# Kernel tuning notes

Hardware: AMD Instinct MI355X
Metric: run time of the kernel (lower is better)

## Reference

```python
import jax, jax.numpy as jnp
import numpy as np

B, F, D = 16384, 32, 64   # batch, n_continuous_features, input_dim
H = 2 * D                  # hidden = 2*input_dim per the d_hidden spec


def setup_inputs() -> dict:
    key = jax.random.key(0)
    ks = jax.random.split(key, 6)
    s1 = 1.0 / np.sqrt(D).astype(np.float32)
    s2 = 1.0 / np.sqrt(H).astype(np.float32)
    return {
        "X": jax.random.normal(ks[0], (B, F), jnp.float32),
        "r_": jax.random.normal(ks[1], (B, F, D), jnp.float32),
        # stacked per-feature weights (one tiny MLP per continuous column)
        "W1": jax.random.normal(ks[2], (F, D, H), jnp.float32) * s1,
        "b1": jax.random.normal(ks[3], (F, H), jnp.float32) * s1,
        "W2": jax.random.normal(ks[4], (F, H, 1), jnp.float32) * s2,
        "b2": jax.random.normal(ks[5], (F, 1), jnp.float32) * s2,
    }


def reference(X, r_, W1, b1, W2, b2):
    # Per-feature 2-layer MLP (Linear->relu->Linear->relu), batched over the
    # feature axis instead of the original Python loop over ModuleDict.
    h = jax.nn.relu(jnp.einsum('bfd,fdh->bfh', r_, W1) + b1)   # [B,F,H]
    y = jax.nn.relu(jnp.einsum('bfh,fho->bfo', h, W2) + b2)    # [B,F,1]
    x = X[..., None]                                           # [B,F,1] raw scalar per column
    # Original returns list of (x_col, mlp_out) pairs; we pack them as [B,F,2]
    # with [...,0]=x and [...,1]=mlp output (same values, dense layout).
    return jnp.concatenate([x, y], axis=-1)
```

## Files before the change

### kernel.cpp

```cpp
#include <hip/hip_runtime.h>
#include <hip/hip_bf16.h>
#include <stdint.h>

#define B_SZ 16384
#define F_SZ 32
#define D_SZ 64
#define H_SZ 128
#define RSTRIDE 72

typedef __attribute__((ext_vector_type(8))) short  short8;
typedef __attribute__((ext_vector_type(4))) float  float4v;
typedef __attribute__((ext_vector_type(4))) unsigned int uint4v;

__device__ __forceinline__ unsigned int pkbf(float lo, float hi) {
  unsigned int ulo = __builtin_bit_cast(unsigned int, lo) + 0x8000u;
  unsigned int uhi = __builtin_bit_cast(unsigned int, hi) + 0x8000u;
  return __builtin_amdgcn_perm(uhi, ulo, 0x07060302u);
}

__global__ __launch_bounds__(256) void ContMlp_prep(
    const float* __restrict__ W1, const float* __restrict__ b1,
    const float* __restrict__ W2, unsigned short* __restrict__ w1t,
    unsigned int* __restrict__ bw) {
  const int f  = blockIdx.x >> 2;
  const int hq = blockIdx.x & 3;
  const int h0 = hq * 32;
  const int t  = threadIdx.x;
  __shared__ float lds[D_SZ][33];
  const float* w1f = W1 + (size_t)f * (D_SZ * H_SZ);
#pragma unroll
  for (int i = 0; i < 8; ++i) {
    int idx = t + 256 * i;
    int d = idx >> 5, hh = idx & 31;
    lds[d][hh] = w1f[d * H_SZ + h0 + hh];
  }
  __syncthreads();
  unsigned short* o = w1t + (size_t)f * (H_SZ * D_SZ);
#pragma unroll
  for (int i = 0; i < 8; ++i) {
    int idx = t + 256 * i;
    int hh = idx >> 6, d = idx & 63;
    unsigned int u = __builtin_bit_cast(unsigned int, lds[d][hh]) + 0x8000u;
    o[(h0 + hh) * D_SZ + d] = (unsigned short)(u >> 16);
  }
  if (hq == 0 && t < H_SZ) {
    unsigned int ub = __builtin_bit_cast(unsigned int, b1[f * H_SZ + t]) + 0x8000u;
    unsigned int uw = __builtin_bit_cast(unsigned int, W2[f * H_SZ + t]) + 0x8000u;
    bw[f * H_SZ + t] = (ub & 0xFFFF0000u) | (uw >> 16);
  }
}

__device__ __forceinline__ void compute_sub(
    float4v c0, float4v c1, float4v c2, float4v c3,
    const unsigned short* w1l, const unsigned int* bwl,
    float b2f, int col, int quad, float* store_ptr) {
  unsigned int p0 = pkbf(c0.x, c0.y), p1 = pkbf(c0.z, c0.w);
  unsigned int p2 = pkbf(c1.x, c1.y), p3 = pkbf(c1.z, c1.w);
  unsigned int p4 = pkbf(c2.x, c2.y), p5 = pkbf(c2.z, c2.w);
  unsigned int p6 = pkbf(c3.x, c3.y), p7 = pkbf(c3.z, c3.w);
  uint4v bq0 = {p0, p1, p2, p3};
  uint4v bq1 = {p4, p5, p6, p7};
  short8 bf0 = __builtin_bit_cast(short8, bq0);
  short8 bf1 = __builtin_bit_cast(short8, bq1);

  float ysum = 0.f;
#pragma unroll
  for (int t = 0; t < 8; ++t) {
    const unsigned short* wrow = w1l + (col + 16 * t) * RSTRIDE + quad * 8;
    short8 a0 = *(const short8*)(wrow);
    short8 a1 = *(const short8*)(wrow + 32);
    float4v acc = {0.f, 0.f, 0.f, 0.f};
    acc = __builtin_amdgcn_mfma_f32_16x16x32_bf16(a0, bf0, acc, 0, 0, 0);
    acc = __builtin_amdgcn_mfma_f32_16x16x32_bf16(a1, bf1, acc, 0, 0, 0);
    uint4v bwv = *(const uint4v*)(bwl + 16 * t + quad * 4);
#pragma unroll
    for (int r = 0; r < 4; ++r) {
      unsigned int u = bwv[r];
      float b1v = __builtin_bit_cast(float, u & 0xFFFF0000u);
      float w2v = __builtin_bit_cast(float, u << 16);
      ysum = fmaf(fmaxf(acc[r] + b1v, 0.f), w2v, ysum);
    }
  }
  ysum += __shfl_xor(ysum, 16, 64);
  ysum += __shfl_xor(ysum, 32, 64);
  float y = fmaxf(ysum + b2f, 0.f);
  if (quad == 0) *store_ptr = y;
}

__global__ void ContMlp_main(
    const float* __restrict__ r_,
    const unsigned short* __restrict__ w1t, const unsigned int* __restrict__ bw,
    const float* __restrict__ b2, float* __restrict__ ydst,
    int y_fmul, int y_rmul, int y_cadd) {
  const int f    = blockIdx.x & 31;
  const int tile = blockIdx.x >> 5;
  const int w    = threadIdx.x >> 6;
  const int l    = threadIdx.x & 63;
  const int col  = l & 15;
  const int quad = l >> 4;

  __shared__ unsigned short w1l[H_SZ * RSTRIDE];
  __shared__ unsigned int   bwl[H_SZ];

  {
    const uint4v* src = (const uint4v*)(w1t + (size_t)f * (H_SZ * D_SZ));
#pragma unroll
    for (int i = 0; i < 4; ++i) {
      int ci = threadIdx.x + 256 * i;
      int h = ci >> 3, dc = ci & 7;
      *(uint4v*)(w1l + h * RSTRIDE + dc * 8) = src[ci];
    }
    if (threadIdx.x < H_SZ) bwl[threadIdx.x] = bw[f * H_SZ + threadIdx.x];
  }
  __syncthreads();
  const float b2f = b2[f];

  const int row_w0 = tile * 256 + w * 64;
  const float* rbase = r_ + (size_t)(row_w0 + col) * (F_SZ * D_SZ)
                          + f * D_SZ + quad * 8;

#define LOADSUB(S, N)                                                   \
  do {                                                                  \
    const float* p_ = rbase + (size_t)(S) * 16 * (F_SZ * D_SZ);         \
    N##0 = *(const float4v*)(p_);      N##1 = *(const float4v*)(p_ + 4);\
    N##2 = *(const float4v*)(p_ + 32); N##3 = *(const float4v*)(p_ + 36);\
  } while (0)

#define YPTR(S) (ydst + (size_t)f * y_fmul                               \
                     + (size_t)(row_w0 + (S)*16 + col) * y_rmul + y_cadd)

  float4v A0, A1, A2, A3, Bb0, Bb1, Bb2, Bb3;
  LOADSUB(0, A);
  LOADSUB(1, Bb);
  compute_sub(A0, A1, A2, A3, w1l, bwl, b2f, col, quad, YPTR(0));
  LOADSUB(2, A);
  compute_sub(Bb0, Bb1, Bb2, Bb3, w1l, bwl, b2f, col, quad, YPTR(1));
  LOADSUB(3, Bb);
  compute_sub(A0, A1, A2, A3, w1l, bwl, b2f, col, quad, YPTR(2));
  compute_sub(Bb0, Bb1, Bb2, Bb3, w1l, bwl, b2f, col, quad, YPTR(3));
#undef LOADSUB
#undef YPTR
}

__global__ __launch_bounds__(256) void ContMlp_combine(
    const float* __restrict__ X, const float* __restrict__ yws,
    float* __restrict__ out) {
  __shared__ float yl[F_SZ][33];
  const int r0 = blockIdx.x * 32;
  const int t = threadIdx.x;
#pragma unroll
  for (int i = 0; i < 4; ++i) {
    int idx = t + 256 * i;
    int f = idx >> 5, r = idx & 31;
    yl[f][r] = yws[(size_t)f * B_SZ + r0 + r];
  }
  __syncthreads();
#pragma unroll
  for (int i = 0; i < 4; ++i) {
    int idx = t + 256 * i;
    int r = idx >> 5, f = idx & 31;
    float2 o2 = make_float2(X[(size_t)(r0 + r) * F_SZ + f], yl[f][r]);
    *(float2*)(out + (size_t)(r0 + r) * (2 * F_SZ) + 2 * f) = o2;
  }
}

__global__ __launch_bounds__(256) void ContMlp_xwrite(
    const float* __restrict__ X, float* __restrict__ out) {
  int idx = blockIdx.x * 256 + threadIdx.x;
  int r = idx >> 5, f = idx & 31;
  out[(size_t)r * (2 * F_SZ) + 2 * f] = X[idx];
}

extern "C" void kernel_launch(void* const* d_in, const int* in_sizes, int n_in,
                              void* d_out, int out_size, void* d_ws, size_t ws_size,
                              hipStream_t stream) {
  const float* X  = (const float*)d_in[0];
  const float* r_ = (const float*)d_in[1];
  const float* W1 = (const float*)d_in[2];
  const float* b1 = (const float*)d_in[3];
  const float* W2 = (const float*)d_in[4];
  const float* b2 = (const float*)d_in[5];
  float* out = (float*)d_out;

  const size_t w1t_bytes = (size_t)F_SZ * H_SZ * D_SZ * 2;
  const size_t bw_off    = w1t_bytes;
  const size_t bw_bytes  = (size_t)F_SZ * H_SZ * 4;
  const size_t y_off     = bw_off + bw_bytes;
  const size_t y_bytes   = (size_t)B_SZ * F_SZ * 4;

  unsigned short* w1t = (unsigned short*)d_ws;
  unsigned int*   bw  = (unsigned int*)((char*)d_ws + bw_off);

  ContMlp_prep<<<F_SZ * 4, 256, 0, stream>>>(W1, b1, W2, w1t, bw);

  const bool pathA = ws_size >= y_off + y_bytes;
  if (pathA) {
    float* yws = (float*)((char*)d_ws + y_off);
    ContMlp_main<<<64 * F_SZ, 256, 0, stream>>>(r_, w1t, bw, b2, yws,
                                                B_SZ, 1, 0);
    ContMlp_combine<<<B_SZ / 32, 256, 0, stream>>>(X, yws, out);
  } else {
    ContMlp_main<<<64 * F_SZ, 256, 0, stream>>>(r_, w1t, bw, b2, out,
                                                2, 2 * F_SZ, 1);
    ContMlp_xwrite<<<(B_SZ * F_SZ) / 256, 256, 0, stream>>>(X, out);
  }
}
```

Baseline: 259.0 us.

## Double the rows per block with a three-deep prefetch ring and nontemporal loads

Each block now handles 512 rows, with 8 sub-tiles per wave instead of 4. This halves the grid and amortizes the per-block LDS staging of the transposed W1. The r_ stream goes through a rotating 3-slot register buffer that prefetches two sub-tiles ahead, uses nontemporal loads, and carries a launch_bounds occupancy hint. The risks are more register pressure and fewer blocks to balance across CUs for a memory-bound stream.

```diff
diff --git a/kernel.cpp b/kernel.cpp
--- a/kernel.cpp
+++ b/kernel.cpp
@@ -51,13 +51,13 @@
 }
 
 __device__ __forceinline__ void compute_sub(
-    float4v c0, float4v c1, float4v c2, float4v c3,
+    const float4v* c,
     const unsigned short* w1l, const unsigned int* bwl,
     float b2f, int col, int quad, float* store_ptr) {
-  unsigned int p0 = pkbf(c0.x, c0.y), p1 = pkbf(c0.z, c0.w);
-  unsigned int p2 = pkbf(c1.x, c1.y), p3 = pkbf(c1.z, c1.w);
-  unsigned int p4 = pkbf(c2.x, c2.y), p5 = pkbf(c2.z, c2.w);
-  unsigned int p6 = pkbf(c3.x, c3.y), p7 = pkbf(c3.z, c3.w);
+  unsigned int p0 = pkbf(c[0].x, c[0].y), p1 = pkbf(c[0].z, c[0].w);
+  unsigned int p2 = pkbf(c[1].x, c[1].y), p3 = pkbf(c[1].z, c[1].w);
+  unsigned int p4 = pkbf(c[2].x, c[2].y), p5 = pkbf(c[2].z, c[2].w);
+  unsigned int p6 = pkbf(c[3].x, c[3].y), p7 = pkbf(c[3].z, c[3].w);
   uint4v bq0 = {p0, p1, p2, p3};
   uint4v bq1 = {p4, p5, p6, p7};
   short8 bf0 = __builtin_bit_cast(short8, bq0);
@@ -87,7 +87,7 @@
   if (quad == 0) *store_ptr = y;
 }
 
-__global__ void ContMlp_main(
+__global__ __launch_bounds__(256, 4) void ContMlp_main(
     const float* __restrict__ r_,
     const unsigned short* __restrict__ w1t, const unsigned int* __restrict__ bw,
     const float* __restrict__ b2, float* __restrict__ ydst,
@@ -115,31 +115,30 @@
   __syncthreads();
   const float b2f = b2[f];
 
-  const int row_w0 = tile * 256 + w * 64;
+  const int row_w0 = tile * 512 + w * 128;
   const float* rbase = r_ + (size_t)(row_w0 + col) * (F_SZ * D_SZ)
                           + f * D_SZ + quad * 8;
 
-#define LOADSUB(S, N)                                                   \
-  do {                                                                  \
-    const float* p_ = rbase + (size_t)(S) * 16 * (F_SZ * D_SZ);         \
-    N##0 = *(const float4v*)(p_);      N##1 = *(const float4v*)(p_ + 4);\
-    N##2 = *(const float4v*)(p_ + 32); N##3 = *(const float4v*)(p_ + 36);\
+  float4v buf[3][4];
+#define LOADSUB(S, BI)                                                      \
+  do {                                                                      \
+    const float* p_ = rbase + (size_t)(S) * 16 * (F_SZ * D_SZ);             \
+    buf[BI][0] = __builtin_nontemporal_load((const float4v*)(p_));          \
+    buf[BI][1] = __builtin_nontemporal_load((const float4v*)(p_ + 4));      \
+    buf[BI][2] = __builtin_nontemporal_load((const float4v*)(p_ + 32));     \
+    buf[BI][3] = __builtin_nontemporal_load((const float4v*)(p_ + 36));     \
   } while (0)
 
-#define YPTR(S) (ydst + (size_t)f * y_fmul                               \
-                     + (size_t)(row_w0 + (S)*16 + col) * y_rmul + y_cadd)
-
-  float4v A0, A1, A2, A3, Bb0, Bb1, Bb2, Bb3;
-  LOADSUB(0, A);
-  LOADSUB(1, Bb);
-  compute_sub(A0, A1, A2, A3, w1l, bwl, b2f, col, quad, YPTR(0));
-  LOADSUB(2, A);
-  compute_sub(Bb0, Bb1, Bb2, Bb3, w1l, bwl, b2f, col, quad, YPTR(1));
-  LOADSUB(3, Bb);
-  compute_sub(A0, A1, A2, A3, w1l, bwl, b2f, col, quad, YPTR(2));
-  compute_sub(Bb0, Bb1, Bb2, Bb3, w1l, bwl, b2f, col, quad, YPTR(3));
+  LOADSUB(0, 0);
+  LOADSUB(1, 1);
+#pragma unroll
+  for (int s = 0; s < 8; ++s) {
+    if (s + 2 < 8) LOADSUB(s + 2, (s + 2) % 3);
+    float* yp = ydst + (size_t)f * y_fmul
+                     + (size_t)(row_w0 + s * 16 + col) * y_rmul + y_cadd;
+    compute_sub(buf[s % 3], w1l, bwl, b2f, col, quad, yp);
+  }
 #undef LOADSUB
-#undef YPTR
 }
 
 __global__ __launch_bounds__(256) void ContMlp_combine(
@@ -196,11 +195,11 @@
   const bool pathA = ws_size >= y_off + y_bytes;
   if (pathA) {
     float* yws = (float*)((char*)d_ws + y_off);
-    ContMlp_main<<<64 * F_SZ, 256, 0, stream>>>(r_, w1t, bw, b2, yws,
+    ContMlp_main<<<32 * F_SZ, 256, 0, stream>>>(r_, w1t, bw, b2, yws,
                                                 B_SZ, 1, 0);
     ContMlp_combine<<<B_SZ / 32, 256, 0, stream>>>(X, yws, out);
   } else {
-    ContMlp_main<<<64 * F_SZ, 256, 0, stream>>>(r_, w1t, bw, b2, out,
+    ContMlp_main<<<32 * F_SZ, 256, 0, stream>>>(r_, w1t, bw, b2, out,
                                                 2, 2 * F_SZ, 1);
     ContMlp_xwrite<<<(B_SZ * F_SZ) / 256, 256, 0, stream>>>(X, out);
   }
```

Result: slower. 264.6 us (+2.1%).
